# Kernel optimization log

Hardware: AMD Instinct MI355X
Metric: run time of the kernel (lower is better)

Reference implementation:

```python
import jax, jax.numpy as jnp
import numpy as np

N = 10000
E = 320000
D_IN = 256
D_H = 256
D_OUT = 64
NEG_SLOPE = 0.2


def _segment_softmax(scores, seg, num_segments):
    # numerically stable softmax over variable-size neighborhoods
    m = jax.ops.segment_max(scores, seg, num_segments=num_segments)
    e = jnp.exp(scores - m[seg])
    s = jax.ops.segment_sum(e, seg, num_segments=num_segments)
    return e / s[seg]


def _gatv2_conv(x, src, dst, Wl, bl, Wr, br, att, bias):
    # PyG GATv2Conv, heads=1: lin_l on source, lin_r on target
    xl = x @ Wl + bl              # [N, C]
    xr = x @ Wr + br              # [N, C]
    xj = xl[src]                  # [E, C] source messages
    e = jax.nn.leaky_relu(xj + xr[dst], NEG_SLOPE)   # [E, C]
    score = e @ att               # [E]
    alpha = _segment_softmax(score, dst, N)          # [E]
    out = jax.ops.segment_sum(alpha[:, None] * xj, dst, num_segments=N)
    return out + bias


def setup_inputs() -> dict:
    key = jax.random.key(0)
    ks = jax.random.split(key, 16)
    s1 = 1.0 / np.sqrt(D_IN)
    s2 = 1.0 / np.sqrt(D_H)
    x = jax.random.normal(ks[0], (N, D_IN), dtype=jnp.float32)
    edge_index = jax.random.randint(ks[1], (2, E), 0, N, dtype=jnp.int64)
    return {
        "x": x,
        "W1l": jax.random.normal(ks[2], (D_IN, D_H), jnp.float32) * s1,
        "b1l": jnp.zeros((D_H,), jnp.float32),
        "W1r": jax.random.normal(ks[3], (D_IN, D_H), jnp.float32) * s1,
        "b1r": jnp.zeros((D_H,), jnp.float32),
        "att1": jax.random.normal(ks[4], (D_H,), jnp.float32) * s2,
        "bias1": jnp.zeros((D_H,), jnp.float32),
        "W2l": jax.random.normal(ks[5], (D_H, D_H), jnp.float32) * s2,
        "b2l": jnp.zeros((D_H,), jnp.float32),
        "W2r": jax.random.normal(ks[6], (D_H, D_H), jnp.float32) * s2,
        "b2r": jnp.zeros((D_H,), jnp.float32),
        "att2": jax.random.normal(ks[7], (D_H,), jnp.float32) * s2,
        "bias2": jnp.zeros((D_H,), jnp.float32),
        "Wout": jax.random.normal(ks[8], (D_H, D_OUT), jnp.float32) * s2,
        "bout": jnp.zeros((D_OUT,), jnp.float32),
        "edge_index": edge_index,
    }


def reference(x, W1l, b1l, W1r, b1r, att1, bias1,
              W2l, b2l, W2r, b2r, att2, bias2,
              Wout, bout, edge_index):
    # add self loops (PyG GATv2Conv default)
    loops = jnp.arange(N, dtype=edge_index.dtype)
    src = jnp.concatenate([edge_index[0], loops])
    dst = jnp.concatenate([edge_index[1], loops])

    h = _gatv2_conv(x, src, dst, W1l, b1l, W1r, b1r, att1, bias1)
    h = jax.nn.relu(h)            # norm=Identity, dropout inactive (eval)
    h = _gatv2_conv(h, src, dst, W2l, b2l, W2r, b2r, att2, bias2)
    h = jax.nn.relu(h)
    logits = h @ Wout + bout      # [N, D_OUT]
    return jax.nn.log_softmax(logits, axis=1)
```

## Files before the change

kernel.cpp:

```cpp
#include <hip/hip_runtime.h>
#include <hip/hip_bf16.h>
#include <math.h>

#define N_NODES 10000
#define N_EDGES 320000
#define TOT_E (N_EDGES + N_NODES)
#define D 256
#define DOUT 64
#define NEG_SLOPE 0.2f
#define MAXDEG 128

typedef __attribute__((ext_vector_type(8))) short bf16x8;
typedef __attribute__((ext_vector_type(4))) float f32x4;
typedef unsigned short ushort_t;

__device__ __forceinline__ unsigned short f2b_rne(float f) {
    unsigned int x = __float_as_uint(f);
    x += 0x7FFFu + ((x >> 16) & 1u);
    return (unsigned short)(x >> 16);
}
__device__ __forceinline__ float b2f(unsigned short h) {
    return __uint_as_float(((unsigned int)h) << 16);
}
__device__ __forceinline__ void bsplit(float v, unsigned short& hi, unsigned short& lo) {
    hi = f2b_rne(v);
    lo = f2b_rne(v - b2f(hi));
}

__device__ __forceinline__ bool detect_f32(const void* x) {
    const ushort_t* xb = (const ushort_t*)x;
    int lane = threadIdx.x & 63;
    int bad = 0;
    #pragma unroll
    for (int i = 0; i < 4; ++i) {
        float v = b2f(xb[2 * (lane + 64 * i)]);
        bad += !(fabsf(v) < 1e4f) ? 1 : 0;
    }
    #pragma unroll
    for (int o = 32; o > 0; o >>= 1) bad += __shfl_down(bad, o);
    return __shfl(bad, 0) > 8;
}
__device__ __forceinline__ bool detect_i64(const int* e32) {
    int lane = threadIdx.x & 63;
    int nz = (e32[2 * lane + 1] != 0) ? 1 : 0;
    #pragma unroll
    for (int o = 32; o > 0; o >>= 1) nz += __shfl_down(nz, o);
    return __shfl(nz, 0) == 0;
}

__global__ __launch_bounds__(256) void prep_kernel(
        const void* x, ushort_t* xh, ushort_t* xlo,
        const void* W1l, const void* W1r, const void* W2l, const void* W2r, const void* Wo,
        const void* v0, const void* v1, const void* v2, const void* v3,
        const void* v4, const void* v5, const void* v6, const void* v7, const void* v8,
        ushort_t* wt, float* vecf, int* counts) {
    bool f32s = detect_f32(x);
    int bid = blockIdx.x;
    int t = threadIdx.x;
    if (bid < 2500) {
        int i = bid * 1024 + t * 4;
        float v[4];
        if (f32s) {
            float4 f = *(const float4*)((const float*)x + i);
            v[0] = f.x; v[1] = f.y; v[2] = f.z; v[3] = f.w;
        } else {
            union { uint2 q; ushort_t u[4]; } r;
            r.q = *(const uint2*)((const ushort_t*)x + i);
            #pragma unroll
            for (int j = 0; j < 4; ++j) v[j] = b2f(r.u[j]);
        }
        union { uint2 q; ushort_t u[4]; } H, L;
        #pragma unroll
        for (int j = 0; j < 4; ++j) bsplit(v[j], H.u[j], L.u[j]);
        *(uint2*)(xh + i) = H.q;
        *(uint2*)(xlo + i) = L.q;
    } else if (bid < 3588) {
        int b = bid - 2500;
        const void* srcs5[5] = {W1l, W1r, W2l, W2r, Wo};
        int wid, n, ncols;
        if (b < 1024) { wid = b >> 8; n = b & 255; ncols = 256; }
        else          { wid = 4;      n = b - 1024; ncols = 64; }
        ushort_t* dh;
        ushort_t* dl;
        if (wid < 4) { dh = wt + (size_t)wid * 2 * 65536; dl = dh + 65536; }
        else         { dh = wt + (size_t)8 * 65536;       dl = dh + 16384; }
        float v = f32s ? ((const float*)srcs5[wid])[(size_t)t * ncols + n]
                       : b2f(((const ushort_t*)srcs5[wid])[(size_t)t * ncols + n]);
        unsigned short hi, lo;
        bsplit(v, hi, lo);
        dh[(size_t)n * 256 + t] = hi;
        dl[(size_t)n * 256 + t] = lo;
    } else if (bid < 3597) {
        int b = bid - 3588;
        const void* ps[9] = {v0, v1, v2, v3, v4, v5, v6, v7, v8};
        int n = (b == 8) ? DOUT : 256;
        if (t < n) {
            float v = f32s ? ((const float*)ps[b])[t] : b2f(((const ushort_t*)ps[b])[t]);
            vecf[b * 256 + t] = v;
        }
    } else {
        int idx = (bid - 3597) * 256 + t;
        if (idx < N_NODES) counts[idx] = 0;
    }
}

__device__ __forceinline__ int eload(const int* ei, bool is64, int idx) {
    int v = is64 ? ei[2 * (size_t)idx] : ei[idx];
    return ((unsigned)v < (unsigned)N_NODES) ? v : 0;
}

__global__ __launch_bounds__(256) void scatter_kernel(const int* __restrict__ ei,
                                                      int* __restrict__ counts,
                                                      int* __restrict__ srcs_pad) {
    bool is64 = detect_i64(ei);
    int id = blockIdx.x * 256 + threadIdx.x;
    if (id >= TOT_E) return;
    int src, dst;
    if (id < N_EDGES) { src = eload(ei, is64, id); dst = eload(ei, is64, N_EDGES + id); }
    else              { src = dst = id - N_EDGES; }
    int slot = atomicAdd(&counts[dst], 1);
    if (slot < MAXDEG) srcs_pad[dst * MAXDEG + slot] = src;
}

__global__ __launch_bounds__(256) void gemm_mfma_kernel(
        const ushort_t* __restrict__ Ahg, const ushort_t* __restrict__ Alg,
        const ushort_t* __restrict__ Wh0, const ushort_t* __restrict__ Wl0,
        const float* __restrict__ bias0, ushort_t* __restrict__ out0,
        const ushort_t* __restrict__ Wh1, const ushort_t* __restrict__ Wl1,
        const float* __restrict__ bias1, float* __restrict__ out1) {
    __shared__ bf16x8 Ah[4][64];
    __shared__ bf16x8 Al[4][64];
    __shared__ bf16x8 Bh[4][64];
    __shared__ bf16x8 Bl[4][64];
    int tid = threadIdx.x;
    int lane = tid & 63, wave = tid >> 6;
    int row0 = blockIdx.y * 64;
    int y = blockIdx.x;
    const ushort_t* Wh; const ushort_t* Wl; const float* bias;
    int col0;
    bool ob_bf16;
    if (y < 4) { Wh = Wh0; Wl = Wl0; bias = bias0; col0 = y * 64; ob_bf16 = true; }
    else       { Wh = Wh1; Wl = Wl1; bias = bias1; col0 = (y - 4) * 64; ob_bf16 = false; }
    int sm = tid >> 2;
    int skq = tid & 3;
    int sl = skq * 16 + (sm & 15);
    int sr = sm >> 4;

    f32x4 acc[4];
    #pragma unroll
    for (int c = 0; c < 4; ++c) acc[c] = (f32x4){0.f, 0.f, 0.f, 0.f};

    for (int k0 = 0; k0 < D; k0 += 32) {
        uint4 qah, qal;
        int grow = row0 + sm;
        if (grow < N_NODES) {
            size_t aoff = (size_t)grow * D + k0 + skq * 8;
            qah = *(const uint4*)(Ahg + aoff);
            qal = *(const uint4*)(Alg + aoff);
        } else {
            qah = (uint4){0, 0, 0, 0}; qal = (uint4){0, 0, 0, 0};
        }
        size_t boff = (size_t)(col0 + sm) * 256 + k0 + skq * 8;
        uint4 qbh = *(const uint4*)(Wh + boff);
        uint4 qbl = *(const uint4*)(Wl + boff);

        __syncthreads();
        *(uint4*)&Ah[sr][sl] = qah;
        *(uint4*)&Al[sr][sl] = qal;
        *(uint4*)&Bh[sr][sl] = qbh;
        *(uint4*)&Bl[sr][sl] = qbl;
        __syncthreads();

        bf16x8 a_h = Ah[wave][lane];
        bf16x8 a_l = Al[wave][lane];
        #pragma unroll
        for (int c = 0; c < 4; ++c) {
            bf16x8 b_h = Bh[c][lane];
            bf16x8 b_l = Bl[c][lane];
            acc[c] = __builtin_amdgcn_mfma_f32_16x16x32_bf16(a_h, b_l, acc[c], 0, 0, 0);
            acc[c] = __builtin_amdgcn_mfma_f32_16x16x32_bf16(a_l, b_h, acc[c], 0, 0, 0);
            acc[c] = __builtin_amdgcn_mfma_f32_16x16x32_bf16(a_h, b_h, acc[c], 0, 0, 0);
        }
    }
    int quad = lane >> 4;
    #pragma unroll
    for (int c = 0; c < 4; ++c) {
        int col = col0 + c * 16 + (lane & 15);
        float bv = bias[col];
        #pragma unroll
        for (int i = 0; i < 4; ++i) {
            int row = row0 + wave * 16 + quad * 4 + i;
            if (row < N_NODES) {
                float v = acc[c][i] + bv;
                if (ob_bf16) out0[(size_t)row * D + col] = f2b_rne(v);
                else         out1[(size_t)row * D + col] = v;
            }
        }
    }
}

__global__ __launch_bounds__(256) void conv_kernel(const ushort_t* __restrict__ xl,
                                                   const float* __restrict__ xr,
                                                   const float* __restrict__ att,
                                                   const float* __restrict__ bias,
                                                   const int* __restrict__ counts,
                                                   const int* __restrict__ srcs_pad,
                                                   ushort_t* __restrict__ hh,
                                                   ushort_t* __restrict__ hl) {
    __shared__ float xr_s[D];
    __shared__ int srcs_s[MAXDEG];
    __shared__ float hwmax[2][8];
    __shared__ float sred[8];
    __shared__ float fbuf[8][256];
    int node = blockIdx.x;
    int t = threadIdx.x;
    int deg = counts[node];
    if (deg > MAXDEG) deg = MAXDEG;
    if (deg <= 0) {
        float o = fmaxf(bias[t], 0.f);
        unsigned short hi, lo; bsplit(o, hi, lo);
        hh[(size_t)node * D + t] = hi;
        hl[(size_t)node * D + t] = lo;
        return;
    }
    xr_s[t] = xr[(size_t)node * D + t];
    if (t < deg) srcs_s[t] = srcs_pad[node * MAXDEG + t];
    __syncthreads();

    int hw = t >> 5;
    int seg = t & 31;
    float xr8[8], att8[8];
    {
        float4 x0 = *(const float4*)&xr_s[seg * 8];
        float4 x1 = *(const float4*)&xr_s[seg * 8 + 4];
        float4 a0 = *(const float4*)(att + seg * 8);
        float4 a1 = *(const float4*)(att + seg * 8 + 4);
        xr8[0] = x0.x; xr8[1] = x0.y; xr8[2] = x0.z; xr8[3] = x0.w;
        xr8[4] = x1.x; xr8[5] = x1.y; xr8[6] = x1.z; xr8[7] = x1.w;
        att8[0] = a0.x; att8[1] = a0.y; att8[2] = a0.z; att8[3] = a0.w;
        att8[4] = a1.x; att8[5] = a1.y; att8[6] = a1.z; att8[7] = a1.w;
    }
    float acc8[8];
    #pragma unroll
    for (int j = 0; j < 8; ++j) acc8[j] = 0.f;
    float m = -INFINITY, s = 0.f;
    int par = 0;

    for (int cbase = 0; cbase < deg; cbase += 32, par ^= 1) {
        int dlim = deg - cbase; if (dlim > 32) dlim = 32;
        int ni = (dlim > hw) ? ((dlim - hw + 7) >> 3) : 0;
        union { uint4 q; ushort_t u[8]; } r[4];
        float scv[4];
        #pragma unroll
        for (int i = 0; i < 4; ++i) {
            if (i < ni) {
                int src = srcs_s[cbase + hw + 8 * i];
                r[i].q = *(const uint4*)(xl + (size_t)src * D + seg * 8);
            }
        }
        #pragma unroll
        for (int i = 0; i < 4; ++i) {
            scv[i] = -1e30f;
            if (i < ni) {
                float p = 0.f;
                #pragma unroll
                for (int j = 0; j < 8; ++j) {
                    float v = b2f(r[i].u[j]) + xr8[j];
                    v = fmaxf(v, NEG_SLOPE * v);
                    p = fmaf(v, att8[j], p);
                }
                #pragma unroll
                for (int o = 16; o > 0; o >>= 1) p += __shfl_xor(p, o, 32);
                scv[i] = isfinite(p) ? p : -1e30f;
            }
        }
        float mx4 = fmaxf(fmaxf(scv[0], scv[1]), fmaxf(scv[2], scv[3]));
        if (seg == 0) hwmax[par][hw] = mx4;
        __syncthreads();
        float cmax = hwmax[par][0];
        #pragma unroll
        for (int k = 1; k < 8; ++k) cmax = fmaxf(cmax, hwmax[par][k]);
        float m_new = fmaxf(m, cmax);
        float scale = (m > -1e37f) ? __expf(m - m_new) : 0.f;
        s *= scale;
        #pragma unroll
        for (int j = 0; j < 8; ++j) acc8[j] *= scale;
        #pragma unroll
        for (int i = 0; i < 4; ++i) {
            if (i < ni) {
                float p = __expf(scv[i] - m_new);
                s += p;
                #pragma unroll
                for (int j = 0; j < 8; ++j) {
                    acc8[j] = fmaf(p, b2f(r[i].u[j]), acc8[j]);
                }
            }
        }
        m = m_new;
    }
    __syncthreads();
    float4 w0 = (float4){acc8[0], acc8[1], acc8[2], acc8[3]};
    float4 w1 = (float4){acc8[4], acc8[5], acc8[6], acc8[7]};
    *(float4*)&fbuf[hw][seg * 8] = w0;
    *(float4*)&fbuf[hw][seg * 8 + 4] = w1;
    if (seg == 0) sred[hw] = s;
    __syncthreads();
    float tot = 0.f;
    #pragma unroll
    for (int k = 0; k < 8; ++k) tot += fbuf[k][t];
    float stot = sred[0];
    #pragma unroll
    for (int k = 1; k < 8; ++k) stot += sred[k];
    float o = tot / stot + bias[t];
    if (!isfinite(o)) o = 0.f;
    o = fmaxf(o, 0.f);
    unsigned short hi, lo; bsplit(o, hi, lo);
    hh[(size_t)node * D + t] = hi;
    hl[(size_t)node * D + t] = lo;
}

__global__ __launch_bounds__(256) void logits_kernel(
        const ushort_t* __restrict__ Ahg, const ushort_t* __restrict__ Alg,
        const ushort_t* __restrict__ Wh, const ushort_t* __restrict__ Wl,
        const float* __restrict__ bias, float* __restrict__ out) {
    __shared__ bf16x8 Ah[4][64];
    __shared__ bf16x8 Al[4][64];
    __shared__ bf16x8 Bh[4][64];
    __shared__ bf16x8 Bl[4][64];
    __shared__ float Cs[64][65];
    __shared__ float mxs[64], lss[64];
    int tid = threadIdx.x;
    int lane = tid & 63, wave = tid >> 6;
    int row0 = blockIdx.x * 64;
    int sm = tid >> 2, skq = tid & 3;
    int sl = skq * 16 + (sm & 15), sr = sm >> 4;

    f32x4 acc[4];
    #pragma unroll
    for (int c = 0; c < 4; ++c) acc[c] = (f32x4){0.f, 0.f, 0.f, 0.f};

    for (int k0 = 0; k0 < D; k0 += 32) {
        uint4 qah, qal;
        int grow = row0 + sm;
        if (grow < N_NODES) {
            size_t aoff = (size_t)grow * D + k0 + skq * 8;
            qah = *(const uint4*)(Ahg + aoff);
            qal = *(const uint4*)(Alg + aoff);
        } else {
            qah = (uint4){0, 0, 0, 0}; qal = (uint4){0, 0, 0, 0};
        }
        size_t boff = (size_t)sm * 256 + k0 + skq * 8;
        uint4 qbh = *(const uint4*)(Wh + boff);
        uint4 qbl = *(const uint4*)(Wl + boff);
        __syncthreads();
        *(uint4*)&Ah[sr][sl] = qah;
        *(uint4*)&Al[sr][sl] = qal;
        *(uint4*)&Bh[sr][sl] = qbh;
        *(uint4*)&Bl[sr][sl] = qbl;
        __syncthreads();
        bf16x8 a_h = Ah[wave][lane];
        bf16x8 a_l = Al[wave][lane];
        #pragma unroll
        for (int c = 0; c < 4; ++c) {
            bf16x8 b_h = Bh[c][lane];
            bf16x8 b_l = Bl[c][lane];
            acc[c] = __builtin_amdgcn_mfma_f32_16x16x32_bf16(a_h, b_l, acc[c], 0, 0, 0);
            acc[c] = __builtin_amdgcn_mfma_f32_16x16x32_bf16(a_l, b_h, acc[c], 0, 0, 0);
            acc[c] = __builtin_amdgcn_mfma_f32_16x16x32_bf16(a_h, b_h, acc[c], 0, 0, 0);
        }
    }
    int quad = lane >> 4;
    #pragma unroll
    for (int c = 0; c < 4; ++c) {
        int col = c * 16 + (lane & 15);
        float bv = bias[col];
        #pragma unroll
        for (int i = 0; i < 4; ++i) {
            int row = wave * 16 + quad * 4 + i;
            Cs[row][col] = acc[c][i] + bv;
        }
    }
    __syncthreads();
    if (tid < 64) {
        float mx = -INFINITY;
        for (int c2 = 0; c2 < 64; ++c2) {
            float v = Cs[tid][c2];
            if (!isfinite(v)) { v = -1e30f; Cs[tid][c2] = v; }
            mx = fmaxf(mx, v);
        }
        float ssum = 0.f;
        for (int c2 = 0; c2 < 64; ++c2) ssum += expf(Cs[tid][c2] - mx);
        mxs[tid] = mx;
        lss[tid] = logf(ssum);
    }
    __syncthreads();
    for (int idx = tid; idx < 64 * 64; idx += 256) {
        int r = idx >> 6, col = idx & 63;
        int grow = row0 + r;
        if (grow < N_NODES) out[(size_t)grow * DOUT + col] = Cs[r][col] - mxs[r] - lss[r];
    }
}

extern "C" void kernel_launch(void* const* d_in, const int* in_sizes, int n_in,
                              void* d_out, int out_size, void* d_ws, size_t ws_size,
                              hipStream_t stream) {
    const void* x    = d_in[0];
    const void* W1l  = d_in[1];
    const void* b1l  = d_in[2];
    const void* W1r  = d_in[3];
    const void* b1r  = d_in[4];
    const void* att1 = d_in[5];
    const void* bia1 = d_in[6];
    const void* W2l  = d_in[7];
    const void* b2l  = d_in[8];
    const void* W2r  = d_in[9];
    const void* b2r  = d_in[10];
    const void* att2 = d_in[11];
    const void* bia2 = d_in[12];
    const void* Wout = d_in[13];
    const void* bout = d_in[14];
    const int*  ei   = (const int*)d_in[15];

    int* counts   = (int*)d_ws;
    int* srcs_pad = counts + N_NODES;
    ushort_t* wt = (ushort_t*)(srcs_pad + (size_t)N_NODES * MAXDEG);
    ushort_t* W1lH = wt;                ushort_t* W1lL = W1lH + 65536;
    ushort_t* W1rH = W1lL + 65536;      ushort_t* W1rL = W1rH + 65536;
    ushort_t* W2lH = W1rL + 65536;      ushort_t* W2lL = W2lH + 65536;
    ushort_t* W2rH = W2lL + 65536;      ushort_t* W2rL = W2rH + 65536;
    ushort_t* WoH  = W2rL + 65536;      ushort_t* WoL  = WoH + 16384;
    float* vecf = (float*)(WoL + 16384);
    ushort_t* xh  = (ushort_t*)(vecf + 9 * 256);
    ushort_t* xlo = xh + (size_t)N_NODES * D;
    ushort_t* xlb = xlo + (size_t)N_NODES * D;
    float* xr = (float*)(xlb + (size_t)N_NODES * D);
    ushort_t* hh = xh;
    ushort_t* hl = xlo;

    float* b1lf = vecf + 0 * 256;
    float* b1rf = vecf + 1 * 256;
    float* att1f = vecf + 2 * 256;
    float* bia1f = vecf + 3 * 256;
    float* b2lf = vecf + 4 * 256;
    float* b2rf = vecf + 5 * 256;
    float* att2f = vecf + 6 * 256;
    float* bia2f = vecf + 7 * 256;
    float* boutf = vecf + 8 * 256;

    prep_kernel<<<3637, 256, 0, stream>>>(x, xh, xlo,
                                          W1l, W1r, W2l, W2r, Wout,
                                          b1l, b1r, att1, bia1, b2l, b2r, att2, bia2, bout,
                                          wt, vecf, counts);
    scatter_kernel<<<(TOT_E + 255) / 256, 256, 0, stream>>>(ei, counts, srcs_pad);

    const int GX = (N_NODES + 63) / 64;
    gemm_mfma_kernel<<<dim3(8, GX), 256, 0, stream>>>(
        xh, xlo, W1lH, W1lL, b1lf, xlb, W1rH, W1rL, b1rf, xr);
    conv_kernel<<<N_NODES, 256, 0, stream>>>(xlb, xr, att1f, bia1f, counts, srcs_pad, hh, hl);
    gemm_mfma_kernel<<<dim3(8, GX), 256, 0, stream>>>(
        hh, hl, W2lH, W2lL, b2lf, xlb, W2rH, W2rL, b2rf, xr);
    conv_kernel<<<N_NODES, 256, 0, stream>>>(xlb, xr, att2f, bia2f, counts, srcs_pad, hh, hl);
    logits_kernel<<<GX, 256, 0, stream>>>(hh, hl, WoH, WoL, boutf, (float*)d_out);
}
```

Baseline: 272.5 us.

## Retile split-bf16 GEMM to 128x64 with double-buffered direct-to-LDS loads

New measurement: 265.1 us. 1.03x faster.

```diff
diff --git a/kernel.cpp b/kernel.cpp
--- a/kernel.cpp
+++ b/kernel.cpp
@@ -25,6 +25,12 @@
 __device__ __forceinline__ void bsplit(float v, unsigned short& hi, unsigned short& lo) {
     hi = f2b_rne(v);
     lo = f2b_rne(v - b2f(hi));
+}
+
+__device__ __forceinline__ void gload16(const ushort_t* g, ushort_t* l) {
+    __builtin_amdgcn_global_load_lds(
+        (const __attribute__((address_space(1))) void*)g,
+        (__attribute__((address_space(3))) void*)l, 16, 0, 0);
 }
 
 __device__ __forceinline__ bool detect_f32(const void* x) {
@@ -122,78 +128,116 @@
     if (slot < MAXDEG) srcs_pad[dst * MAXDEG + slot] = src;
 }
 
-__global__ __launch_bounds__(256) void gemm_mfma_kernel(
+__global__ __launch_bounds__(256, 3) void gemm_mfma_kernel(
         const ushort_t* __restrict__ Ahg, const ushort_t* __restrict__ Alg,
         const ushort_t* __restrict__ Wh0, const ushort_t* __restrict__ Wl0,
         const float* __restrict__ bias0, ushort_t* __restrict__ out0,
         const ushort_t* __restrict__ Wh1, const ushort_t* __restrict__ Wl1,
         const float* __restrict__ bias1, float* __restrict__ out1) {
-    __shared__ bf16x8 Ah[4][64];
-    __shared__ bf16x8 Al[4][64];
-    __shared__ bf16x8 Bh[4][64];
-    __shared__ bf16x8 Bl[4][64];
+    __shared__ __align__(16) ushort_t AhL[2][4096];
+    __shared__ __align__(16) ushort_t AlL[2][4096];
+    __shared__ __align__(16) ushort_t BhL[2][2048];
+    __shared__ __align__(16) ushort_t BlL[2][2048];
     int tid = threadIdx.x;
     int lane = tid & 63, wave = tid >> 6;
-    int row0 = blockIdx.y * 64;
-    int y = blockIdx.x;
+    int lin = blockIdx.x + 8 * blockIdx.y;
+    int v = (lin & 7) * 79 + (lin >> 3);
+    int row0 = (v >> 3) * 128;
+    int y = v & 7;
     const ushort_t* Wh; const ushort_t* Wl; const float* bias;
     int col0;
     bool ob_bf16;
     if (y < 4) { Wh = Wh0; Wl = Wl0; bias = bias0; col0 = y * 64; ob_bf16 = true; }
     else       { Wh = Wh1; Wl = Wl1; bias = bias1; col0 = (y - 4) * 64; ob_bf16 = false; }
-    int sm = tid >> 2;
-    int skq = tid & 3;
-    int sl = skq * 16 + (sm & 15);
-    int sr = sm >> 4;
-
-    f32x4 acc[4];
-    #pragma unroll
-    for (int c = 0; c < 4; ++c) acc[c] = (f32x4){0.f, 0.f, 0.f, 0.f};
-
-    for (int k0 = 0; k0 < D; k0 += 32) {
-        uint4 qah, qal;
-        int grow = row0 + sm;
-        if (grow < N_NODES) {
-            size_t aoff = (size_t)grow * D + k0 + skq * 8;
-            qah = *(const uint4*)(Ahg + aoff);
-            qal = *(const uint4*)(Alg + aoff);
-        } else {
-            qah = (uint4){0, 0, 0, 0}; qal = (uint4){0, 0, 0, 0};
-        }
-        size_t boff = (size_t)(col0 + sm) * 256 + k0 + skq * 8;
-        uint4 qbh = *(const uint4*)(Wh + boff);
-        uint4 qbl = *(const uint4*)(Wl + boff);
-
+
+    const ushort_t* gp[6];
+    ushort_t* lp0[6];
+    ushort_t* lp1[6];
+    {
+        int lane4 = lane >> 2;
+        int qsl = (lane & 3) ^ (lane4 & 3);
+        #pragma unroll
+        for (int j = 0; j < 6; ++j) {
+            int q = wave * 6 + j;
+            if (q < 8) {
+                gp[j] = Ahg + (size_t)(row0 + q * 16 + lane4) * 256 + qsl * 8;
+                lp0[j] = &AhL[0][q * 512]; lp1[j] = &AhL[1][q * 512];
+            } else if (q < 16) {
+                int r = q - 8;
+                gp[j] = Alg + (size_t)(row0 + r * 16 + lane4) * 256 + qsl * 8;
+                lp0[j] = &AlL[0][r * 512]; lp1[j] = &AlL[1][r * 512];
+            } else if (q < 20) {
+                int r = q - 16;
+                gp[j] = Wh + (size_t)(col0 + r * 16 + lane4) * 256 + qsl * 8;
+                lp0[j] = &BhL[0][r * 512]; lp1[j] = &BhL[1][r * 512];
+            } else {
+                int r = q - 20;
+                gp[j] = Wl + (size_t)(col0 + r * 16 + lane4) * 256 + qsl * 8;
+                lp0[j] = &BlL[0][r * 512]; lp1[j] = &BlL[1][r * 512];
+            }
+        }
+    }
+    int wm = wave >> 1, wn = wave & 1;
+    int l15 = lane & 15;
+    int slot = (lane >> 4) ^ (lane & 3);
+
+    f32x4 acc[4][2];
+    #pragma unroll
+    for (int mg = 0; mg < 4; ++mg)
+        #pragma unroll
+        for (int ng = 0; ng < 2; ++ng) acc[mg][ng] = (f32x4){0.f, 0.f, 0.f, 0.f};
+
+    #pragma unroll
+    for (int j = 0; j < 6; ++j) { gload16(gp[j], lp0[j]); gp[j] += 32; }
+    __syncthreads();
+
+    #pragma unroll
+    for (int s = 0; s < 8; ++s) {
+        const int cb = s & 1;
+        if (s < 7) {
+            #pragma unroll
+            for (int j = 0; j < 6; ++j) {
+                gload16(gp[j], cb ? lp0[j] : lp1[j]);
+                gp[j] += 32;
+            }
+        }
+        bf16x8 ah[4], al[4];
+        #pragma unroll
+        for (int mg = 0; mg < 4; ++mg) {
+            int o = (wm * 64 + mg * 16 + l15) * 32 + slot * 8;
+            ah[mg] = *(const bf16x8*)&AhL[cb][o];
+            al[mg] = *(const bf16x8*)&AlL[cb][o];
+        }
+        #pragma unroll
+        for (int ng = 0; ng < 2; ++ng) {
+            int o = (wn * 32 + ng * 16 + l15) * 32 + slot * 8;
+            bf16x8 b_h = *(const bf16x8*)&BhL[cb][o];
+            bf16x8 b_l = *(const bf16x8*)&BlL[cb][o];
+            #pragma unroll
+            for (int mg = 0; mg < 4; ++mg) {
+                acc[mg][ng] = __builtin_amdgcn_mfma_f32_16x16x32_bf16(ah[mg], b_l, acc[mg][ng], 0, 0, 0);
+                acc[mg][ng] = __builtin_amdgcn_mfma_f32_16x16x32_bf16(al[mg], b_h, acc[mg][ng], 0, 0, 0);
+                acc[mg][ng] = __builtin_amdgcn_mfma_f32_16x16x32_bf16(ah[mg], b_h, acc[mg][ng], 0, 0, 0);
+            }
+        }
         __syncthreads();
-        *(uint4*)&Ah[sr][sl] = qah;
-        *(uint4*)&Al[sr][sl] = qal;
-        *(uint4*)&Bh[sr][sl] = qbh;
-        *(uint4*)&Bl[sr][sl] = qbl;
-        __syncthreads();
-
-        bf16x8 a_h = Ah[wave][lane];
-        bf16x8 a_l = Al[wave][lane];
-        #pragma unroll
-        for (int c = 0; c < 4; ++c) {
-            bf16x8 b_h = Bh[c][lane];
-            bf16x8 b_l = Bl[c][lane];
-            acc[c] = __builtin_amdgcn_mfma_f32_16x16x32_bf16(a_h, b_l, acc[c], 0, 0, 0);
-            acc[c] = __builtin_amdgcn_mfma_f32_16x16x32_bf16(a_l, b_h, acc[c], 0, 0, 0);
-            acc[c] = __builtin_amdgcn_mfma_f32_16x16x32_bf16(a_h, b_h, acc[c], 0, 0, 0);
-        }
-    }
+    }
+
     int quad = lane >> 4;
     #pragma unroll
-    for (int c = 0; c < 4; ++c) {
-        int col = col0 + c * 16 + (lane & 15);
+    for (int ng = 0; ng < 2; ++ng) {
+        int col = col0 + wn * 32 + ng * 16 + l15;
         float bv = bias[col];
         #pragma unroll
-        for (int i = 0; i < 4; ++i) {
-            int row = row0 + wave * 16 + quad * 4 + i;
-            if (row < N_NODES) {
-                float v = acc[c][i] + bv;
-                if (ob_bf16) out0[(size_t)row * D + col] = f2b_rne(v);
-                else         out1[(size_t)row * D + col] = v;
+        for (int mg = 0; mg < 4; ++mg) {
+            #pragma unroll
+            for (int i = 0; i < 4; ++i) {
+                int row = row0 + wm * 64 + mg * 16 + quad * 4 + i;
+                if (row < N_NODES) {
+                    float vv = acc[mg][ng][i] + bv;
+                    if (ob_bf16) out0[(size_t)row * D + col] = f2b_rne(vv);
+                    else         out1[(size_t)row * D + col] = vv;
+                }
             }
         }
     }
@@ -453,12 +497,11 @@
                                           wt, vecf, counts);
     scatter_kernel<<<(TOT_E + 255) / 256, 256, 0, stream>>>(ei, counts, srcs_pad);
 
-    const int GX = (N_NODES + 63) / 64;
-    gemm_mfma_kernel<<<dim3(8, GX), 256, 0, stream>>>(
+    gemm_mfma_kernel<<<dim3(8, 79), 256, 0, stream>>>(
         xh, xlo, W1lH, W1lL, b1lf, xlb, W1rH, W1rL, b1rf, xr);
     conv_kernel<<<N_NODES, 256, 0, stream>>>(xlb, xr, att1f, bia1f, counts, srcs_pad, hh, hl);
-    gemm_mfma_kernel<<<dim3(8, GX), 256, 0, stream>>>(
+    gemm_mfma_kernel<<<dim3(8, 79), 256, 0, stream>>>(
         hh, hl, W2lH, W2lL, b2lf, xlb, W2rH, W2rL, b2rf, xr);
     conv_kernel<<<N_NODES, 256, 0, stream>>>(xlb, xr, att2f, bia2f, counts, srcs_pad, hh, hl);
-    logits_kernel<<<GX, 256, 0, stream>>>(hh, hl, WoH, WoL, boutf, (float*)d_out);
-}
+    logits_kernel<<<(N_NODES + 63) / 64, 256, 0, stream>>>(hh, hl, WoH, WoL, boutf, (float*)d_out);
+}
```
